# Kernel tuning notes

Measured on AMD Instinct MI355X. Metric: run time of the kernel, lower is better.

The kernel has to match this reference:

```python
import jax, jax.numpy as jnp
import numpy as np

H = W = 128      # image_shape
B = 64           # batch_size
O = 32           # orbit_size
RADIANS = True   # args.radians
RADIAN_INIT = 1.57
AFFINE_INIT = 0.1


def setup_inputs() -> dict:
    key = jax.random.key(0)
    k1, k2 = jax.random.split(key)
    X = jax.random.normal(k1, (B, H * W), dtype=jnp.float32)
    eps = jax.random.uniform(k2, (O, 7), dtype=jnp.float32)
    base = np.array([3.14, 1.0, 1.0, 1.0, 1.0, 1.0, 1.0], np.float32)
    ident = np.array([RADIAN_INIT, 1.0, 1.0, 0.0, 0.0, 0.0, 0.0], np.float32)
    tmin = ident - AFFINE_INIT * base
    tmax = np.array([-RADIAN_INIT, 1.0, 1.0, 0.0, 0.0, 0.0, 0.0], np.float32) + AFFINE_INIT * base
    return {
        "X": X,
        "eps": eps,
        "theta_min": jnp.asarray(tmin)[None, :],
        "theta_max": jnp.asarray(tmax)[None, :],
    }


def _affine_entries(thetas):
    # thetas: [O, 7] = [angle, sx, sy, shear_x, shear_y, tx, ty]
    # A = R(angle) @ [[sx, px], [py, sy]]  (rotation * scale/shear), t = [tx, ty]
    ang, sx, sy, px, py, tx, ty = (thetas[:, i] for i in range(7))
    if not RADIANS:
        ang = ang * (np.pi / 180.0)
    c, s = jnp.cos(ang), jnp.sin(ang)
    a00 = c * sx - s * py
    a01 = c * px - s * sy
    a10 = s * sx + c * py
    a11 = s * px + c * sy
    return a00, a01, a10, a11, tx, ty


def reference(X, eps, theta_min, theta_max):
    # sample orbit thetas: [O, 7]
    thetas = theta_min + (theta_max - theta_min) * eps
    a00, a01, a10, a11, tx, ty = _affine_entries(thetas)

    imgs = X.reshape(-1, H, W)  # [B, H, W]

    # normalized sampling grid in [-1, 1]
    xg = jnp.linspace(-1.0, 1.0, W, dtype=X.dtype)
    yg = jnp.linspace(-1.0, 1.0, H, dtype=X.dtype)
    Yg, Xg = jnp.meshgrid(yg, xg, indexing="ij")  # [H, W]

    # affine-transformed source coords per orbit sample: [O, H, W]
    xs = a00[:, None, None] * Xg + a01[:, None, None] * Yg + tx[:, None, None]
    ys = a10[:, None, None] * Xg + a11[:, None, None] * Yg + ty[:, None, None]

    # to pixel coords (align-corners convention)
    x = (xs + 1.0) * (W - 1) * 0.5
    y = (ys + 1.0) * (H - 1) * 0.5

    x0f = jnp.floor(x)
    y0f = jnp.floor(y)
    wx = x - x0f
    wy = y - y0f
    x0 = jnp.clip(x0f.astype(jnp.int32), 0, W - 1)
    x1 = jnp.clip(x0f.astype(jnp.int32) + 1, 0, W - 1)
    y0 = jnp.clip(y0f.astype(jnp.int32), 0, H - 1)
    y1 = jnp.clip(y0f.astype(jnp.int32) + 1, 0, H - 1)

    # gather 4 corners: fancy index over all images at once -> [B, O, H, W]
    Ia = imgs[:, y0, x0]
    Ib = imgs[:, y1, x0]
    Ic = imgs[:, y0, x1]
    Id = imgs[:, y1, x1]

    wa = (1.0 - wx) * (1.0 - wy)
    wb = (1.0 - wx) * wy
    wc = wx * (1.0 - wy)
    wd = wx * wy

    out = Ia * wa + Ib * wb + Ic * wc + Id * wd  # [B, O, H, W]
    out = jnp.transpose(out, (1, 0, 2, 3))       # [O, B, H, W]: per-theta batches
    return out.reshape(B * O, H, W, 1)
```

## Files before the change

### kernel.cpp

```cpp
#include <hip/hip_runtime.h>

#define HH 128
#define WW 128
#define BB 64
#define OO 32

__global__ void coeff_kernel(const float* __restrict__ eps,
                             const float* __restrict__ tmin,
                             const float* __restrict__ tmax,
                             float* __restrict__ coef) {
    int o = threadIdx.x;
    if (o >= OO) return;
    float th[7];
#pragma unroll
    for (int i = 0; i < 7; ++i) {
        float mn = tmin[i], mx = tmax[i];
        th[i] = mn + (mx - mn) * eps[o * 7 + i];
    }
    float ang = th[0], sx = th[1], sy = th[2], px = th[3], py = th[4], tx = th[5], ty = th[6];
    float c = cosf(ang), s = sinf(ang);
    float a00 = c * sx - s * py;
    float a01 = c * px - s * sy;
    float a10 = s * sx + c * py;
    float a11 = s * px + c * sy;
    const float half = 0.5f * (WW - 1);
    coef[o * 8 + 0] = a00 * half;
    coef[o * 8 + 1] = a01 * half;
    coef[o * 8 + 2] = (tx + 1.0f) * half;
    coef[o * 8 + 3] = a10 * half;
    coef[o * 8 + 4] = a11 * half;
    coef[o * 8 + 5] = (ty + 1.0f) * half;
}

__launch_bounds__(256, 1)
__global__ void sample_kernel(const float* __restrict__ X,
                              const float* __restrict__ coef,
                              float* __restrict__ out) {
    __shared__ float img[HH * WW];

    const int bid = blockIdx.x;
    const int o   = bid & (OO - 1);
    const int b   = bid >> 5;
    const int tid = threadIdx.x;

    {
        const float4* __restrict__ src = (const float4*)(X + b * (HH * WW));
        float4* dst = (float4*)img;
#pragma unroll
        for (int i = 0; i < 16; ++i)
            dst[tid + i * 256] = src[tid + i * 256];
    }

    const float cx0 = coef[o * 8 + 0];
    const float cx1 = coef[o * 8 + 1];
    const float cxt = coef[o * 8 + 2];
    const float cy0 = coef[o * 8 + 3];
    const float cy1 = coef[o * 8 + 4];
    const float cyt = coef[o * 8 + 5];

    __syncthreads();

    const int w  = tid & (WW - 1);
    const int h0 = tid >> 7;
    const float step = 2.0f / 127.0f;
    const float Xg = -1.0f + w * step;
    const float bxw = fmaf(cx0, Xg, cxt);
    const float byw = fmaf(cy0, Xg, cyt);

    float* __restrict__ outp = out + ((size_t)(o * BB + b) * (HH * WW)) + w;

#pragma unroll 8
    for (int i = 0; i < 64; ++i) {
        const int h = h0 + i * 2;
        const float Yg = -1.0f + h * step;
        const float x = fmaf(cx1, Yg, bxw);
        const float y = fmaf(cy1, Yg, byw);

        const float x0f = floorf(x);
        const float y0f = floorf(y);
        const float wx = x - x0f;
        const float wy = y - y0f;
        const int ix = (int)x0f;
        const int iy = (int)y0f;
        const int x0 = min(max(ix, 0), WW - 1);
        const int x1 = min(max(ix + 1, 0), WW - 1);
        const int y0 = min(max(iy, 0), HH - 1);
        const int y1 = min(max(iy + 1, 0), HH - 1);

        const int r0 = y0 << 7;
        const int r1 = y1 << 7;
        const float Ia = img[r0 + x0];
        const float Ic = img[r0 + x1];
        const float Ib = img[r1 + x0];
        const float Id = img[r1 + x1];

        const float owx = 1.0f - wx;
        const float owy = 1.0f - wy;
        const float top = fmaf(Ic, wx, Ia * owx);
        const float bot = fmaf(Id, wx, Ib * owx);
        outp[h * WW] = fmaf(bot, wy, top * owy);
    }
}

extern "C" void kernel_launch(void* const* d_in, const int* in_sizes, int n_in,
                              void* d_out, int out_size, void* d_ws, size_t ws_size,
                              hipStream_t stream) {
    const float* X    = (const float*)d_in[0];
    const float* eps  = (const float*)d_in[1];
    const float* tmin = (const float*)d_in[2];
    const float* tmax = (const float*)d_in[3];
    float* out  = (float*)d_out;
    float* coef = (float*)d_ws;

    coeff_kernel<<<1, 64, 0, stream>>>(eps, tmin, tmax, coef);

    const int nblocks = OO * BB;
    sample_kernel<<<nblocks, 256, 0, stream>>>(X, coef, out);
}
```

Before: 172.4 us.

## Reuse shared image tile across four orbit samples per block and simplify clamping

Each block now loads one image into shared memory and computes four orbit transforms from it, instead of one. This cuts the repeated global-to-LDS image loads by four and launches fewer, larger blocks of 512 threads. The per-pixel index clamping is replaced by clamping the float coordinate to [0, 127), which removes the integer min/max work and lets the four corners be addressed with fixed offsets. The lerp is also rewritten in a shorter fma form. The float clamp gives slightly different values than the original at the far image edge, and the larger blocks change occupancy.

```diff
diff --git a/kernel.cpp b/kernel.cpp
--- a/kernel.cpp
+++ b/kernel.cpp
@@ -32,73 +32,71 @@
     coef[o * 8 + 5] = (ty + 1.0f) * half;
 }
 
-__launch_bounds__(256, 1)
+__launch_bounds__(512)
 __global__ void sample_kernel(const float* __restrict__ X,
                               const float* __restrict__ coef,
                               float* __restrict__ out) {
     __shared__ float img[HH * WW];
 
     const int bid = blockIdx.x;
-    const int o   = bid & (OO - 1);
-    const int b   = bid >> 5;
+    const int og  = bid & 7;
+    const int b   = bid >> 3;
     const int tid = threadIdx.x;
 
     {
         const float4* __restrict__ src = (const float4*)(X + b * (HH * WW));
         float4* dst = (float4*)img;
 #pragma unroll
-        for (int i = 0; i < 16; ++i)
-            dst[tid + i * 256] = src[tid + i * 256];
+        for (int i = 0; i < 8; ++i)
+            dst[tid + i * 512] = src[tid + i * 512];
     }
-
-    const float cx0 = coef[o * 8 + 0];
-    const float cx1 = coef[o * 8 + 1];
-    const float cxt = coef[o * 8 + 2];
-    const float cy0 = coef[o * 8 + 3];
-    const float cy1 = coef[o * 8 + 4];
-    const float cyt = coef[o * 8 + 5];
-
     __syncthreads();
 
     const int w  = tid & (WW - 1);
     const int h0 = tid >> 7;
     const float step = 2.0f / 127.0f;
     const float Xg = -1.0f + w * step;
-    const float bxw = fmaf(cx0, Xg, cxt);
-    const float byw = fmaf(cy0, Xg, cyt);
+    const float hi = 126.999992f;
 
-    float* __restrict__ outp = out + ((size_t)(o * BB + b) * (HH * WW)) + w;
+#pragma unroll
+    for (int j = 0; j < 4; ++j) {
+        const int o = og * 4 + j;
+        const float cx0 = coef[o * 8 + 0];
+        const float cx1 = coef[o * 8 + 1];
+        const float cxt = coef[o * 8 + 2];
+        const float cy0 = coef[o * 8 + 3];
+        const float cy1 = coef[o * 8 + 4];
+        const float cyt = coef[o * 8 + 5];
+
+        const float bxw = fmaf(cx0, Xg, cxt);
+        const float byw = fmaf(cy0, Xg, cyt);
+
+        float* __restrict__ outp = out + ((size_t)(o * BB + b) * (HH * WW)) + w;
 
 #pragma unroll 8
-    for (int i = 0; i < 64; ++i) {
-        const int h = h0 + i * 2;
-        const float Yg = -1.0f + h * step;
-        const float x = fmaf(cx1, Yg, bxw);
-        const float y = fmaf(cy1, Yg, byw);
+        for (int i = 0; i < 32; ++i) {
+            const int h = h0 + i * 4;
+            const float Yg = -1.0f + h * step;
+            float x = fmaf(cx1, Yg, bxw);
+            float y = fmaf(cy1, Yg, byw);
+            x = fminf(fmaxf(x, 0.0f), hi);
+            y = fminf(fmaxf(y, 0.0f), hi);
 
-        const float x0f = floorf(x);
-        const float y0f = floorf(y);
-        const float wx = x - x0f;
-        const float wy = y - y0f;
-        const int ix = (int)x0f;
-        const int iy = (int)y0f;
-        const int x0 = min(max(ix, 0), WW - 1);
-        const int x1 = min(max(ix + 1, 0), WW - 1);
-        const int y0 = min(max(iy, 0), HH - 1);
-        const int y1 = min(max(iy + 1, 0), HH - 1);
+            const float x0f = floorf(x);
+            const float y0f = floorf(y);
+            const float wx = x - x0f;
+            const float wy = y - y0f;
+            const int idx = ((int)y0f << 7) + (int)x0f;
 
-        const int r0 = y0 << 7;
-        const int r1 = y1 << 7;
-        const float Ia = img[r0 + x0];
-        const float Ic = img[r0 + x1];
-        const float Ib = img[r1 + x0];
-        const float Id = img[r1 + x1];
+            const float Ia = img[idx];
+            const float Ic = img[idx + 1];
+            const float Ib = img[idx + WW];
+            const float Id = img[idx + WW + 1];
 
-        const float owx = 1.0f - wx;
-        const float owy = 1.0f - wy;
-        const float top = fmaf(Ic, wx, Ia * owx);
-        const float bot = fmaf(Id, wx, Ib * owx);
-        outp[h * WW] = fmaf(bot, wy, top * owy);
+            const float top = fmaf(wx, Ic - Ia, Ia);
+            const float bot = fmaf(wx, Id - Ib, Ib);
+            outp[h * WW] = fmaf(wy, bot - top, top);
+        }
     }
 }
 
@@ -114,6 +112,6 @@
 
     coeff_kernel<<<1, 64, 0, stream>>>(eps, tmin, tmax, coef);
 
-    const int nblocks = OO * BB;
-    sample_kernel<<<nblocks, 256, 0, stream>>>(X, coef, out);
+    const int nblocks = BB * 8;
+    sample_kernel<<<nblocks, 512, 0, stream>>>(X, coef, out);
 }
```

After: 158.3 us. -8.2%, faster.
